# Performance work log

Measured on AMD Instinct MI355X. Metric: run time of the kernel, lower is better.

## Reference

```python
import jax, jax.numpy as jnp
import numpy as np

N_HEAD, D_MODEL, D_HEAD, D_OUT = 16, 1024, 64, 1024
Q_INNER = N_HEAD * D_HEAD


def setup_inputs() -> dict:
    key = jax.random.key(0)
    ks = jax.random.split(key, 10)
    B, S = 1, 4096
    hidden_state = jax.random.normal(ks[0], (B, S, D_MODEL), dtype=jnp.float32)
    # causal mask, (B,1,S,S), 1 = attend, 0 = masked
    attention_mask = jnp.tril(jnp.ones((S, S), dtype=jnp.int32))[None, None, :, :]
    s = 0.02
    Wq = jax.random.normal(ks[1], (D_MODEL, Q_INNER), dtype=jnp.float32) * s
    bq = jnp.zeros((Q_INNER,), dtype=jnp.float32)
    Wk = jax.random.normal(ks[2], (D_MODEL, D_HEAD), dtype=jnp.float32) * s
    bk = jnp.zeros((D_HEAD,), dtype=jnp.float32)
    Wv = jax.random.normal(ks[3], (D_MODEL, D_HEAD), dtype=jnp.float32) * s
    bv = jnp.zeros((D_HEAD,), dtype=jnp.float32)
    Wo = jax.random.normal(ks[4], (Q_INNER, D_OUT), dtype=jnp.float32) * s
    bo = jnp.zeros((D_OUT,), dtype=jnp.float32)
    return {"hidden_state": hidden_state, "attention_mask": attention_mask,
            "Wq": Wq, "bq": bq, "Wk": Wk, "bk": bk, "Wv": Wv, "bv": bv,
            "Wo": Wo, "bo": bo}


def reference(hidden_state, attention_mask, Wq, bq, Wk, bk, Wv, bv, Wo, bo):
    B, S, _ = hidden_state.shape
    q = hidden_state @ Wq + bq                    # (B,S,H*Dh)
    k = hidden_state @ Wk + bk                    # (B,S,Dh) single shared KV head
    v = hidden_state @ Wv + bv                    # (B,S,Dh)
    q = q.reshape(B, S, N_HEAD, D_HEAD)           # (B,S,H,Dh)
    scale = 1.0 / jnp.sqrt(jnp.float32(D_HEAD))
    # scores: (B,H,S,S) — shared K broadcast over heads
    scores = jnp.einsum('bqhd,bkd->bhqk', q, k) * scale
    scores = jnp.where(attention_mask == 0, -jnp.inf, scores)
    probs = jax.nn.softmax(scores, axis=-1)
    out = jnp.einsum('bhqk,bkd->bqhd', probs, v)  # (B,S,H,Dh)
    out = out.reshape(B, S, Q_INNER)
    return out @ Wo + bo
```

## Files before the change

### kernel.cpp

```cpp
#include <hip/hip_runtime.h>
#include <hip/hip_bf16.h>
#include <math.h>

typedef __bf16 bf16;
typedef __bf16 bf16x4 __attribute__((ext_vector_type(4)));
typedef __bf16 bf16x8 __attribute__((ext_vector_type(8)));
typedef float f32x4 __attribute__((ext_vector_type(4)));

#define AS1(p) ((const __attribute__((address_space(1))) void*)(p))
#define AS3(p) ((__attribute__((address_space(3))) void*)(p))

__device__ __forceinline__ void gld_lds16(const void* g, void* l) {
  __builtin_amdgcn_global_load_lds(AS1(g), AS3(l), 16, 0, 0);
}

#define MFMA16(a, b, c) __builtin_amdgcn_mfma_f32_16x16x32_bf16((a), (b), (c), 0, 0, 0)

#define QSCALE_F 0.180336880f


struct Sched { unsigned short e[768]; };
constexpr Sched make_sched() {
  Sched s{};
  for (int bx = 0; bx < 256; ++bx) {
    int h = bx >> 4, i = bx & 15;
    s.e[bx]       = (unsigned short)(((31 - i) << 6) | (h << 2) | 1);
    s.e[bx + 256] = (unsigned short)(((31 - i) << 6) | (h << 2) | 2);
    s.e[bx + 512] = (unsigned short)((i << 6) | (h << 2) | 0);
  }
  return s;
}
__device__ constexpr Sched SCHED = make_sched();

__global__ void cast_f32_bf16_sw(const float4* __restrict__ in, bf16* __restrict__ out,
                                 int n4) {
  int i = blockIdx.x * blockDim.x + threadIdx.x;
  if (i < n4) {
    float4 v = in[i];
    bf16x4 o4 = {(bf16)v.x, (bf16)v.y, (bf16)v.z, (bf16)v.w};
    const int e = i * 4;
    const int row = e >> 10;
    const int idx = (e & ~63) | ((e & 63) ^ ((row & 7) << 3));
    *(bf16x4*)(out + (size_t)idx) = o4;
  }
}

__global__ void prep_wqkv(const float* __restrict__ Wq, const float* __restrict__ Wk,
                          const float* __restrict__ Wv, bf16* __restrict__ out) {
  __shared__ float t[64][65];
  const int ob = blockIdx.y;
  const float* src;
  int C, c0;
  if (ob < 16)      { src = Wq; C = 1024; c0 = ob * 64; }
  else if (ob == 16){ src = Wk; C = 64;   c0 = 0; }
  else              { src = Wv; C = 64;   c0 = 0; }
  const int r0 = blockIdx.x * 64;
  const int tx = threadIdx.x & 63, ty = threadIdx.x >> 6;
#pragma unroll
  for (int j = 0; j < 16; j++)
    t[ty + j * 4][tx] = src[(size_t)(r0 + ty + j * 4) * C + c0 + tx];
  __syncthreads();
#pragma unroll
  for (int j = 0; j < 16; j++) {
    const int orow = ob * 64 + ty + j * 4;
    out[(size_t)orow * 1024 + r0 + (tx ^ ((orow & 7) << 3))] = (bf16)t[tx][ty + j * 4];
  }
}

__global__ void transpose_cast_sw(const float* __restrict__ in, bf16* __restrict__ out,
                                  int C, int ldout) {
  __shared__ float t[64][65];
  int r0 = blockIdx.y * 64, c0 = blockIdx.x * 64;
  int tx = threadIdx.x & 63, ty = threadIdx.x >> 6;
#pragma unroll
  for (int j = 0; j < 16; j++)
    t[ty + j * 4][tx] = in[(size_t)(r0 + ty + j * 4) * C + c0 + tx];
  __syncthreads();
#pragma unroll
  for (int j = 0; j < 16; j++) {
    const int orow = c0 + ty + j * 4;
    out[(size_t)orow * ldout + r0 + (tx ^ ((orow & 7) << 3))] = (bf16)t[tx][ty + j * 4];
  }
}

__global__ void pack_bias3(const float* __restrict__ bq, const float* __restrict__ bk,
                           const float* __restrict__ bv, float* __restrict__ o) {
  int i = blockIdx.x * 256 + threadIdx.x;
  if (i < 1024) o[i] = bq[i];
  else if (i < 1088) o[i] = bk[i - 1024];
  else if (i < 1152) o[i] = bv[i - 1088];
}

template <int OUTF32, int QSCALE>
__global__ __launch_bounds__(256) void gemm_bt64k(const bf16* __restrict__ A,
                                                  const bf16* __restrict__ B,
                                                  const float* __restrict__ bias,
                                                  void* __restrict__ Cout,
                                                  int M, int N, int K) {
  __shared__ bf16 As[2 * 64 * 64];
  __shared__ bf16 Bs[2 * 128 * 64];
  const int tid = threadIdx.x, w = tid >> 6, lane = tid & 63;
  const int g = lane >> 4, r = lane & 15;
  const int cpx = gridDim.x >> 3;
  const int l = (blockIdx.x & 7) * cpx + (blockIdx.x >> 3);
  const int ntn = N >> 7;
  const int my = l / ntn, mx = l - my * ntn;
  const int tm = my * 64, tn = mx * 128;
  const int wr = w >> 1, wc = w & 1;
  const int sz = (r & 7) << 4;

  f32x4 acc[2][4] = {};

  const char* gA = (const char*)(A + (size_t)tm * K);
  const char* gB = (const char*)(B + (size_t)tn * K);
  const int linA0 = (w * 2 + 0) * 1024 + lane * 16;
  const int linA1 = (w * 2 + 1) * 1024 + lane * 16;
  const int linB0 = (w * 4 + 0) * 1024 + lane * 16;
  const int linB1 = (w * 4 + 1) * 1024 + lane * 16;
  const int linB2 = (w * 4 + 2) * 1024 + lane * 16;
  const int linB3 = (w * 4 + 3) * 1024 + lane * 16;

  auto STAGE = [&](int ks, int b) {
    char* dA = (char*)As + b * 8192 + (w * 2) * 1024;
    char* dB = (char*)Bs + b * 16384 + (w * 4) * 1024;
    gld_lds16(gA + (size_t)(linA0 >> 7) * (K * 2) + ks * 128 + (linA0 & 127), dA);
    gld_lds16(gA + (size_t)(linA1 >> 7) * (K * 2) + ks * 128 + (linA1 & 127), dA + 1024);
    gld_lds16(gB + (size_t)(linB0 >> 7) * (K * 2) + ks * 128 + (linB0 & 127), dB);
    gld_lds16(gB + (size_t)(linB1 >> 7) * (K * 2) + ks * 128 + (linB1 & 127), dB + 1024);
    gld_lds16(gB + (size_t)(linB2 >> 7) * (K * 2) + ks * 128 + (linB2 & 127), dB + 2048);
    gld_lds16(gB + (size_t)(linB3 >> 7) * (K * 2) + ks * 128 + (linB3 & 127), dB + 3072);
  };

  const int nk = K >> 6;
  STAGE(0, 0);
  int buf = 0;
  for (int ks = 0; ks < nk; ++ks) {
    if (ks + 1 < nk) {
      STAGE(ks + 1, buf ^ 1);
      asm volatile("s_waitcnt vmcnt(6)" ::: "memory");
    } else {
      asm volatile("s_waitcnt vmcnt(0)" ::: "memory");
    }
    __builtin_amdgcn_sched_barrier(0);
    __builtin_amdgcn_s_barrier();

    const char* at = (const char*)As + buf * 8192;
    const char* bt = (const char*)Bs + buf * 16384;
    bf16x8 af[2][2], bfr[4][2];
#pragma unroll
    for (int m = 0; m < 2; m++)
#pragma unroll
      for (int kk = 0; kk < 2; kk++)
        af[m][kk] = *(const bf16x8*)(at + (wr * 32 + m * 16 + r) * 128 +
                                     ((kk * 64 + g * 16) ^ sz));
#pragma unroll
    for (int n = 0; n < 4; n++)
#pragma unroll
      for (int kk = 0; kk < 2; kk++)
        bfr[n][kk] = *(const bf16x8*)(bt + (wc * 64 + n * 16 + r) * 128 +
                                      ((kk * 64 + g * 16) ^ sz));
    __builtin_amdgcn_s_setprio(1);
#pragma unroll
    for (int m = 0; m < 2; m++)
#pragma unroll
      for (int n = 0; n < 4; n++) {
        acc[m][n] = MFMA16(af[m][0], bfr[n][0], acc[m][n]);
        acc[m][n] = MFMA16(af[m][1], bfr[n][1], acc[m][n]);
      }
    __builtin_amdgcn_s_setprio(0);
    __builtin_amdgcn_s_barrier();
    buf ^= 1;
  }

#pragma unroll
  for (int m = 0; m < 2; m++) {
#pragma unroll
    for (int n = 0; n < 4; n++) {
      int crow = tm + wr * 32 + m * 16 + g * 4;
      int ccol = tn + wc * 64 + n * 16 + r;
      float bb = bias[ccol];
      float sc = (QSCALE && ccol < 1024) ? QSCALE_F : 1.0f;
#pragma unroll
      for (int j = 0; j < 4; j++) {
        float v = (acc[m][n][j] + bb) * sc;
        if (OUTF32)
          ((float*)Cout)[(size_t)(crow + j) * N + ccol] = v;
        else
          ((bf16*)Cout)[(size_t)(crow + j) * N + ccol] = (bf16)v;
      }
    }
  }
}

__global__ void kv_prep(const bf16* __restrict__ QKV, bf16* __restrict__ Ksw,
                        bf16* __restrict__ Vtsw) {
  __shared__ bf16 Vld[64][72];
  const int kv0 = blockIdx.x * 64;
  const int tid = threadIdx.x;
#pragma unroll
  for (int cc = 0; cc < 2; cc++) {
    const int c = tid + cc * 256;
    const int kvl = c >> 3, c8 = c & 7;
    bf16x8 kv8 = *(const bf16x8*)(QKV + (size_t)(kv0 + kvl) * 1152 + 1024 + c8 * 8);
    *(bf16x8*)(Ksw + (size_t)(kv0 + kvl) * 64 + ((c8 * 8) ^ ((kvl & 7) << 3))) = kv8;
    bf16x8 vv = *(const bf16x8*)(QKV + (size_t)(kv0 + kvl) * 1152 + 1088 + c8 * 8);
#pragma unroll
    for (int e = 0; e < 8; e++) Vld[c8 * 8 + e][kvl] = vv[e];
  }
  __syncthreads();
#pragma unroll
  for (int cc = 0; cc < 2; cc++) {
    const int c = tid + cc * 256;
    const int d = c >> 3, k8 = c & 7;
    bf16x8 o8 = *(const bf16x8*)&Vld[d][k8 * 8];
    *(bf16x8*)(Vtsw + (size_t)d * 4096 + kv0 + ((k8 * 8) ^ ((d & 7) << 3))) = o8;
  }
}

__global__ __launch_bounds__(256) void mqa_fwd(const bf16* __restrict__ QKV,
                                               const bf16* __restrict__ Ksw,
                                               const bf16* __restrict__ Vtsw,
                                               bf16* __restrict__ AO,
                                               float* __restrict__ po,
                                               float* __restrict__ psum) {
  __shared__ bf16 Ks[2][64 * 64];
  __shared__ bf16 Vs[2][64 * 64];
  __shared__ bf16 Ps[4 * 32 * 64];

  const int e = SCHED.e[blockIdx.x];
  const int qt = e >> 6, h = (e >> 2) & 15, part = e & 3;
  const int tbeg = (part == 2) ? qt + 1 : 0;
  const int tend = (part == 1) ? qt + 1 : 2 * qt + 2;

  const int tid = threadIdx.x, w = tid >> 6, lane = tid & 63;
  const int g = lane >> 4, r = lane & 15;
  const int qw = qt * 128 + w * 32;
  const int qown0 = qw + r;
  const int qown1 = qw + 16 + r;

  const char* Kg = (const char*)Ksw;
  const char* Vg = (const char*)Vtsw;
  char* PsB = (char*)Ps;
  const int lin0 = w * 2048 + lane * 16;
  const int lin1 = lin0 + 1024;
  const int sz = (r & 7) << 4;

  bf16x8 qf0[2], qf1[2];
#pragma unroll
  for (int kk = 0; kk < 2; kk++) {
    qf0[kk] = *(const bf16x8*)&QKV[(size_t)qown0 * 1152 + h * 64 + kk * 32 + g * 8];
    qf1[kk] = *(const bf16x8*)&QKV[(size_t)qown1 * 1152 + h * 64 + kk * 32 + g * 8];
  }

  const bf16 one = (bf16)1.0f;
  const bf16x8 ones = {one, one, one, one, one, one, one, one};

  f32x4 o[2][4] = {};
  f32x4 sums[2] = {};

  auto STAGE = [&](int t, int b) {
    const int kn = t * 64;
    char* kb = (char*)Ks + b * 8192 + w * 2048;
    char* vb = (char*)Vs + b * 8192 + w * 2048;
    gld_lds16(Kg + (size_t)kn * 128 + lin0, kb);
    gld_lds16(Kg + (size_t)kn * 128 + lin1, kb + 1024);
    gld_lds16(Vg + (size_t)(lin0 >> 7) * 8192 + kn * 2 + (lin0 & 127), vb);
    gld_lds16(Vg + (size_t)(lin1 >> 7) * 8192 + kn * 2 + (lin1 & 127), vb + 1024);
  };

  int buf = 0;
  STAGE(tbeg, 0);
  for (int t = tbeg; t < tend; ++t) {
    if (t + 1 < tend) {
      STAGE(t + 1, buf ^ 1);
      asm volatile("s_waitcnt vmcnt(4)" ::: "memory");
    } else {
      asm volatile("s_waitcnt vmcnt(0)" ::: "memory");
    }
    __builtin_amdgcn_sched_barrier(0);
    __builtin_amdgcn_s_barrier();

    const char* kt = (const char*)Ks + buf * 8192;
    const char* vt = (const char*)Vs + buf * 8192;
    const int kv0 = t * 64;

    f32x4 s0[4], s1[4];
    __builtin_amdgcn_s_setprio(1);
#pragma unroll
    for (int n = 0; n < 4; n++) {
      bf16x8 kf0 = *(const bf16x8*)(kt + (n * 16 + r) * 128 + ((g * 16) ^ sz));
      bf16x8 kf1 = *(const bf16x8*)(kt + (n * 16 + r) * 128 + ((64 + g * 16) ^ sz));
      f32x4 z0 = {0.f, 0.f, 0.f, 0.f};
      z0 = MFMA16(kf0, qf0[0], z0);
      z0 = MFMA16(kf1, qf0[1], z0);
      s0[n] = z0;
      f32x4 z1 = {0.f, 0.f, 0.f, 0.f};
      z1 = MFMA16(kf0, qf1[0], z1);
      z1 = MFMA16(kf1, qf1[1], z1);
      s1[n] = z1;
    }
    __builtin_amdgcn_s_setprio(0);

    if (t >= 2 * qt) {
#pragma unroll
      for (int n = 0; n < 4; n++)
#pragma unroll
        for (int jj = 0; jj < 4; jj++) {
          const int kv = kv0 + n * 16 + g * 4 + jj;
          if (kv > qown0) s0[n][jj] = -3.0e38f;
          if (kv > qown1) s1[n][jj] = -3.0e38f;
        }
    }

#pragma unroll
    for (int n = 0; n < 4; n++) {
      bf16x4 pk0, pk1;
#pragma unroll
      for (int jj = 0; jj < 4; jj++) {
        pk0[jj] = (bf16)__builtin_amdgcn_exp2f(s0[n][jj]);
        pk1[jj] = (bf16)__builtin_amdgcn_exp2f(s1[n][jj]);
      }
      *(bf16x4*)(PsB + w * 4096 + r * 128 + ((n * 32 + g * 8) ^ sz)) = pk0;
      *(bf16x4*)(PsB + w * 4096 + (16 + r) * 128 + ((n * 32 + g * 8) ^ sz)) = pk1;
    }

    asm volatile("s_waitcnt lgkmcnt(0)" ::: "memory");
    __builtin_amdgcn_sched_barrier(0);

    bf16x8 pa00 = *(const bf16x8*)(PsB + w * 4096 + r * 128 + ((g * 16) ^ sz));
    bf16x8 pa01 = *(const bf16x8*)(PsB + w * 4096 + r * 128 + ((64 + g * 16) ^ sz));
    bf16x8 pa10 = *(const bf16x8*)(PsB + w * 4096 + (16 + r) * 128 + ((g * 16) ^ sz));
    bf16x8 pa11 = *(const bf16x8*)(PsB + w * 4096 + (16 + r) * 128 + ((64 + g * 16) ^ sz));
    __builtin_amdgcn_s_setprio(1);
    sums[0] = MFMA16(pa00, ones, sums[0]);
    sums[0] = MFMA16(pa01, ones, sums[0]);
    sums[1] = MFMA16(pa10, ones, sums[1]);
    sums[1] = MFMA16(pa11, ones, sums[1]);
#pragma unroll
    for (int n = 0; n < 4; n++) {
      bf16x8 vf0 = *(const bf16x8*)(vt + (n * 16 + r) * 128 + ((g * 16) ^ sz));
      bf16x8 vf1 = *(const bf16x8*)(vt + (n * 16 + r) * 128 + ((64 + g * 16) ^ sz));
      o[0][n] = MFMA16(pa00, vf0, o[0][n]);
      o[0][n] = MFMA16(pa01, vf1, o[0][n]);
      o[1][n] = MFMA16(pa10, vf0, o[1][n]);
      o[1][n] = MFMA16(pa11, vf1, o[1][n]);
    }
    __builtin_amdgcn_s_setprio(0);
    __builtin_amdgcn_s_barrier();
    buf ^= 1;
  }

  if (part == 0) {
#pragma unroll
    for (int H = 0; H < 2; H++)
#pragma unroll
      for (int jj = 0; jj < 4; jj++) {
        const float inv = 1.f / sums[H][jj];
        const int row = qw + H * 16 + g * 4 + jj;
        const int key = (row & 7) << 3;
#pragma unroll
        for (int n = 0; n < 4; n++)
          AO[(size_t)row * 1024 + h * 64 + ((n * 16 + r) ^ key)] =
              (bf16)(o[H][n][jj] * inv);
      }
  } else {
    const int slot = ((qt - 16) * 16 + h) * 2 + (part - 1);
    float* pb = po + (size_t)slot * 8192;
#pragma unroll
    for (int H = 0; H < 2; H++)
#pragma unroll
      for (int jj = 0; jj < 4; jj++) {
        const int row = w * 32 + H * 16 + g * 4 + jj;
#pragma unroll
        for (int n = 0; n < 4; n++)
          pb[row * 64 + n * 16 + r] = o[H][n][jj];
        if (r == 0) psum[slot * 128 + row] = sums[H][jj];
      }
  }
}

__global__ __launch_bounds__(256) void combine_split(const float* __restrict__ po,
                                                     const float* __restrict__ psum,
                                                     bf16* __restrict__ AO) {
  const int bxx = blockIdx.x;
  const int qt = 16 + (bxx >> 4), h = bxx & 15;
  const float* a  = po + (size_t)bxx * 16384;
  const float* b  = a + 8192;
  const float* sa = psum + bxx * 256;
  const float* sb = sa + 128;
  const int row = threadIdx.x >> 1, c0 = (threadIdx.x & 1) * 32;
  const float inv = 1.f / (sa[row] + sb[row]);
  const float* pa = a + row * 64 + c0;
  const float* pb = b + row * 64 + c0;
  const int grow = qt * 128 + row;
  const int key = (grow & 7) << 3;
  bf16* dst = AO + (size_t)grow * 1024 + h * 64;
#pragma unroll
  for (int i = 0; i < 8; i++) {
    float4 va = ((const float4*)pa)[i];
    float4 vb = ((const float4*)pb)[i];
    bf16x4 o4 = {(bf16)((va.x + vb.x) * inv), (bf16)((va.y + vb.y) * inv),
                 (bf16)((va.z + vb.z) * inv), (bf16)((va.w + vb.w) * inv)};
    *(bf16x4*)(dst + ((c0 + i * 4) ^ key)) = o4;
  }
}

extern "C" void kernel_launch(void* const* d_in, const int* in_sizes, int n_in,
                              void* d_out, int out_size, void* d_ws, size_t ws_size,
                              hipStream_t stream) {
  const float* H  = (const float*)d_in[0];
  const float* Wq = (const float*)d_in[2];
  const float* bq = (const float*)d_in[3];
  const float* Wk = (const float*)d_in[4];
  const float* bk = (const float*)d_in[5];
  const float* Wv = (const float*)d_in[6];
  const float* bv = (const float*)d_in[7];
  const float* Wo = (const float*)d_in[8];
  const float* bo = (const float*)d_in[9];
  float* out = (float*)d_out;

  const int S = 4096, DM = 1024;

  char* p = (char*)d_ws;
  bf16* Hb    = (bf16*)(p);
  bf16* QKV   = (bf16*)(p + 8388608);
  bf16* Wqkvt = (bf16*)(p + 17825792);
  bf16* Wot   = (bf16*)(p + 20185088);
  float* bqkv = (float*)(p + 22282240);
  bf16* Ksw   = (bf16*)(p + 22286848);
  bf16* Vtsw  = (bf16*)(p + 22811136);
  float* po   = (float*)(p + 23335424);
  float* psum = (float*)(p + 40112640);
  bf16* AOb   = Hb;

  cast_f32_bf16_sw<<<(S * DM / 4 + 255) / 256, 256, 0, stream>>>((const float4*)H, Hb,
                                                                 S * DM / 4);
  prep_wqkv<<<dim3(16, 18), 256, 0, stream>>>(Wq, Wk, Wv, Wqkvt);
  transpose_cast_sw<<<dim3(16, 16), 256, 0, stream>>>(Wo, Wot, 1024, 1024);
  pack_bias3<<<5, 256, 0, stream>>>(bq, bk, bv, bqkv);

  gemm_bt64k<0, 1><<<576, 256, 0, stream>>>(Hb, Wqkvt, bqkv, QKV, S, 1152, 1024);

  kv_prep<<<64, 256, 0, stream>>>(QKV, Ksw, Vtsw);

  mqa_fwd<<<768, 256, 0, stream>>>(QKV, Ksw, Vtsw, AOb, po, psum);
  combine_split<<<256, 256, 0, stream>>>(po, psum, AOb);

  gemm_bt64k<1, 0><<<512, 256, 0, stream>>>(AOb, Wot, bo, out, S, 1024, 1024);
}
```

Before: 118.2 us.

## Balance causal attention work with variable-length KV splits and bf16 partials

Replaces the fixed two-way split of the upper query tiles with a compile-time work tape that cuts every (query tile, head) row into chunks of at most 22 KV tiles, ordered longest first. This gives 1008 blocks of more even size so the GPU tail at the end of the grid is shorter. The combine kernel now sums a variable number of partial outputs per tile. Those partials are stored as bf16 instead of fp32 to halve their traffic, which costs some accuracy in the unnormalized partial sums.

```diff
diff --git a/kernel.cpp b/kernel.cpp
--- a/kernel.cpp
+++ b/kernel.cpp
@@ -19,18 +19,48 @@
 #define QSCALE_F 0.180336880f
 
 
-struct Sched { unsigned short e[768]; };
-constexpr Sched make_sched() {
-  Sched s{};
-  for (int bx = 0; bx < 256; ++bx) {
-    int h = bx >> 4, i = bx & 15;
-    s.e[bx]       = (unsigned short)(((31 - i) << 6) | (h << 2) | 1);
-    s.e[bx + 256] = (unsigned short)(((31 - i) << 6) | (h << 2) | 2);
-    s.e[bx + 512] = (unsigned short)((i << 6) | (h << 2) | 0);
-  }
-  return s;
-}
-__device__ constexpr Sched SCHED = make_sched();
+struct Seg { short qt, h, t0, t1, slot; };
+struct Tape { Seg s[1008]; };
+struct CJob { short qt, h, base, parts; };
+struct CTab { CJob j[336]; };
+
+constexpr int nparts_of(int qt) { int T = 2 * qt + 2; return (T + 21) / 22; }
+constexpr int slot_base(int h, int qt) {
+  int b = h * 52;
+  if (qt <= 21) return b + (qt - 11) * 2;
+  return b + 22 + (qt - 22) * 3;
+}
+
+constexpr Tape make_tape() {
+  Tape tp{};
+  int idx = 0;
+  for (int s = 22; s >= 1; --s)
+    for (int h = 0; h < 16; ++h)
+      for (int qt = 0; qt < 32; ++qt) {
+        const int T = 2 * qt + 2, P = nparts_of(qt);
+        for (int p = 0; p < P; ++p) {
+          const int a = p * T / P, b = (p + 1) * T / P;
+          if (b - a == s) {
+            const int slot = (P == 1) ? -1 : slot_base(h, qt) + p;
+            tp.s[idx++] = Seg{(short)qt, (short)h, (short)a, (short)b, (short)slot};
+          }
+        }
+      }
+  return tp;
+}
+
+constexpr CTab make_ctab() {
+  CTab ct{};
+  int n = 0;
+  for (int h = 0; h < 16; ++h)
+    for (int qt = 11; qt < 32; ++qt)
+      ct.j[n++] = CJob{(short)qt, (short)h, (short)slot_base(h, qt),
+                       (short)nparts_of(qt)};
+  return ct;
+}
+
+__device__ constexpr Tape TAPE = make_tape();
+__device__ constexpr CTab CTAB = make_ctab();
 
 __global__ void cast_f32_bf16_sw(const float4* __restrict__ in, bf16* __restrict__ out,
                                  int n4) {
@@ -221,16 +251,14 @@
                                                const bf16* __restrict__ Ksw,
                                                const bf16* __restrict__ Vtsw,
                                                bf16* __restrict__ AO,
-                                               float* __restrict__ po,
+                                               bf16* __restrict__ po,
                                                float* __restrict__ psum) {
   __shared__ bf16 Ks[2][64 * 64];
   __shared__ bf16 Vs[2][64 * 64];
   __shared__ bf16 Ps[4 * 32 * 64];
 
-  const int e = SCHED.e[blockIdx.x];
-  const int qt = e >> 6, h = (e >> 2) & 15, part = e & 3;
-  const int tbeg = (part == 2) ? qt + 1 : 0;
-  const int tend = (part == 1) ? qt + 1 : 2 * qt + 2;
+  const Seg sg = TAPE.s[blockIdx.x];
+  const int qt = sg.qt, h = sg.h, tbeg = sg.t0, tend = sg.t1, slot = sg.slot;
 
   const int tid = threadIdx.x, w = tid >> 6, lane = tid & 63;
   const int g = lane >> 4, r = lane & 15;
@@ -350,7 +378,7 @@
     buf ^= 1;
   }
 
-  if (part == 0) {
+  if (slot < 0) {
 #pragma unroll
     for (int H = 0; H < 2; H++)
 #pragma unroll
@@ -364,8 +392,7 @@
               (bf16)(o[H][n][jj] * inv);
       }
   } else {
-    const int slot = ((qt - 16) * 16 + h) * 2 + (part - 1);
-    float* pb = po + (size_t)slot * 8192;
+    bf16* pb = po + (size_t)slot * 8192;
 #pragma unroll
     for (int H = 0; H < 2; H++)
 #pragma unroll
@@ -373,34 +400,38 @@
         const int row = w * 32 + H * 16 + g * 4 + jj;
 #pragma unroll
         for (int n = 0; n < 4; n++)
-          pb[row * 64 + n * 16 + r] = o[H][n][jj];
+          pb[row * 64 + n * 16 + r] = (bf16)o[H][n][jj];
         if (r == 0) psum[slot * 128 + row] = sums[H][jj];
       }
   }
 }
 
-__global__ __launch_bounds__(256) void combine_split(const float* __restrict__ po,
+__global__ __launch_bounds__(256) void combine_split(const bf16* __restrict__ po,
                                                      const float* __restrict__ psum,
                                                      bf16* __restrict__ AO) {
-  const int bxx = blockIdx.x;
-  const int qt = 16 + (bxx >> 4), h = bxx & 15;
-  const float* a  = po + (size_t)bxx * 16384;
-  const float* b  = a + 8192;
-  const float* sa = psum + bxx * 256;
-  const float* sb = sa + 128;
+  const CJob cj = CTAB.j[blockIdx.x];
   const int row = threadIdx.x >> 1, c0 = (threadIdx.x & 1) * 32;
-  const float inv = 1.f / (sa[row] + sb[row]);
-  const float* pa = a + row * 64 + c0;
-  const float* pb = b + row * 64 + c0;
-  const int grow = qt * 128 + row;
+  float acc[32] = {};
+  float ssum = 0.f;
+#pragma unroll 1
+  for (int p = 0; p < cj.parts; ++p) {
+    const bf16* pb = po + (size_t)(cj.base + p) * 8192 + row * 64 + c0;
+    ssum += psum[(cj.base + p) * 128 + row];
+#pragma unroll
+    for (int v = 0; v < 4; ++v) {
+      bf16x8 x = ((const bf16x8*)pb)[v];
+#pragma unroll
+      for (int e = 0; e < 8; e++) acc[v * 8 + e] += (float)x[e];
+    }
+  }
+  const float inv = 1.f / ssum;
+  const int grow = cj.qt * 128 + row;
   const int key = (grow & 7) << 3;
-  bf16* dst = AO + (size_t)grow * 1024 + h * 64;
+  bf16* dst = AO + (size_t)grow * 1024 + cj.h * 64;
 #pragma unroll
   for (int i = 0; i < 8; i++) {
-    float4 va = ((const float4*)pa)[i];
-    float4 vb = ((const float4*)pb)[i];
-    bf16x4 o4 = {(bf16)((va.x + vb.x) * inv), (bf16)((va.y + vb.y) * inv),
-                 (bf16)((va.z + vb.z) * inv), (bf16)((va.w + vb.w) * inv)};
+    bf16x4 o4 = {(bf16)(acc[i * 4 + 0] * inv), (bf16)(acc[i * 4 + 1] * inv),
+                 (bf16)(acc[i * 4 + 2] * inv), (bf16)(acc[i * 4 + 3] * inv)};
     *(bf16x4*)(dst + ((c0 + i * 4) ^ key)) = o4;
   }
 }
@@ -429,8 +460,8 @@
   float* bqkv = (float*)(p + 22282240);
   bf16* Ksw   = (bf16*)(p + 22286848);
   bf16* Vtsw  = (bf16*)(p + 22811136);
-  float* po   = (float*)(p + 23335424);
-  float* psum = (float*)(p + 40112640);
+  bf16* po    = (bf16*)(p + 23335424);
+  float* psum = (float*)(p + 36966912);
   bf16* AOb   = Hb;
 
   cast_f32_bf16_sw<<<(S * DM / 4 + 255) / 256, 256, 0, stream>>>((const float4*)H, Hb,
@@ -443,8 +474,8 @@
 
   kv_prep<<<64, 256, 0, stream>>>(QKV, Ksw, Vtsw);
 
-  mqa_fwd<<<768, 256, 0, stream>>>(QKV, Ksw, Vtsw, AOb, po, psum);
-  combine_split<<<256, 256, 0, stream>>>(po, psum, AOb);
+  mqa_fwd<<<1008, 256, 0, stream>>>(QKV, Ksw, Vtsw, AOb, po, psum);
+  combine_split<<<336, 256, 0, stream>>>(po, psum, AOb);
 
   gemm_bt64k<1, 0><<<512, 256, 0, stream>>>(AOb, Wot, bo, out, S, 1024, 1024);
 }
```

Measured after the change: 119.9 us. Within noise of the previous version (+1.5%).

## Feed P from registers into K=16 MFMA, dropping LDS round-trip for probabilities

Applied to the files above, without the earlier changes.

Replaces the LDS write/read of the softmax probabilities with a register-resident path. The 16x16x32 MFMA output layout is consumed directly as the A operand of the 16x16x16 bf16_1k MFMA. This removes the Ps shared buffer, one waitcnt/sched barrier and per-tile LDS traffic, and reduces LDS footprint so launch_bounds can request 3 blocks per SIMD. In exchange it issues twice as many MFMA instructions, each with half the K, and loads V fragments in smaller 4-element pieces, which adds register pressure.

```diff
diff --git a/kernel.cpp b/kernel.cpp
--- a/kernel.cpp
+++ b/kernel.cpp
@@ -6,6 +6,7 @@
 typedef __bf16 bf16x4 __attribute__((ext_vector_type(4)));
 typedef __bf16 bf16x8 __attribute__((ext_vector_type(8)));
 typedef float f32x4 __attribute__((ext_vector_type(4)));
+typedef short s16x4 __attribute__((ext_vector_type(4)));
 
 #define AS1(p) ((const __attribute__((address_space(1))) void*)(p))
 #define AS3(p) ((__attribute__((address_space(3))) void*)(p))
@@ -15,6 +16,7 @@
 }
 
 #define MFMA16(a, b, c) __builtin_amdgcn_mfma_f32_16x16x32_bf16((a), (b), (c), 0, 0, 0)
+#define MFMA16K(a, b, c) __builtin_amdgcn_mfma_f32_16x16x16bf16_1k((a), (b), (c), 0, 0, 0)
 
 #define QSCALE_F 0.180336880f
 
@@ -217,15 +219,14 @@
   }
 }
 
-__global__ __launch_bounds__(256) void mqa_fwd(const bf16* __restrict__ QKV,
-                                               const bf16* __restrict__ Ksw,
-                                               const bf16* __restrict__ Vtsw,
-                                               bf16* __restrict__ AO,
-                                               float* __restrict__ po,
-                                               float* __restrict__ psum) {
+__global__ __launch_bounds__(256, 3) void mqa_fwd(const bf16* __restrict__ QKV,
+                                                  const bf16* __restrict__ Ksw,
+                                                  const bf16* __restrict__ Vtsw,
+                                                  bf16* __restrict__ AO,
+                                                  float* __restrict__ po,
+                                                  float* __restrict__ psum) {
   __shared__ bf16 Ks[2][64 * 64];
   __shared__ bf16 Vs[2][64 * 64];
-  __shared__ bf16 Ps[4 * 32 * 64];
 
   const int e = SCHED.e[blockIdx.x];
   const int qt = e >> 6, h = (e >> 2) & 15, part = e & 3;
@@ -240,7 +241,6 @@
 
   const char* Kg = (const char*)Ksw;
   const char* Vg = (const char*)Vtsw;
-  char* PsB = (char*)Ps;
   const int lin0 = w * 2048 + lane * 16;
   const int lin1 = lin0 + 1024;
   const int sz = (r & 7) << 4;
@@ -252,11 +252,9 @@
     qf1[kk] = *(const bf16x8*)&QKV[(size_t)qown1 * 1152 + h * 64 + kk * 32 + g * 8];
   }
 
-  const bf16 one = (bf16)1.0f;
-  const bf16x8 ones = {one, one, one, one, one, one, one, one};
-
   f32x4 o[2][4] = {};
   f32x4 sums[2] = {};
+  const s16x4 ones4 = {0x3F80, 0x3F80, 0x3F80, 0x3F80};
 
   auto STAGE = [&](int t, int b) {
     const int kn = t * 64;
@@ -301,6 +299,14 @@
     }
     __builtin_amdgcn_s_setprio(0);
 
+    s16x4 vf[4][4];
+#pragma unroll
+    for (int kb = 0; kb < 4; kb++)
+#pragma unroll
+      for (int n = 0; n < 4; n++)
+        vf[kb][n] = *(const s16x4*)(vt + (n * 16 + r) * 128 +
+                                    ((kb * 32 + g * 8) ^ sz));
+
     if (t >= 2 * qt) {
 #pragma unroll
       for (int n = 0; n < 4; n++)
@@ -312,38 +318,26 @@
         }
     }
 
-#pragma unroll
-    for (int n = 0; n < 4; n++) {
-      bf16x4 pk0, pk1;
+    union PW { bf16x4 hh; s16x4 ss; };
+    PW p0[4], p1[4];
+#pragma unroll
+    for (int n = 0; n < 4; n++)
 #pragma unroll
       for (int jj = 0; jj < 4; jj++) {
-        pk0[jj] = (bf16)__builtin_amdgcn_exp2f(s0[n][jj]);
-        pk1[jj] = (bf16)__builtin_amdgcn_exp2f(s1[n][jj]);
-      }
-      *(bf16x4*)(PsB + w * 4096 + r * 128 + ((n * 32 + g * 8) ^ sz)) = pk0;
-      *(bf16x4*)(PsB + w * 4096 + (16 + r) * 128 + ((n * 32 + g * 8) ^ sz)) = pk1;
-    }
-
-    asm volatile("s_waitcnt lgkmcnt(0)" ::: "memory");
-    __builtin_amdgcn_sched_barrier(0);
-
-    bf16x8 pa00 = *(const bf16x8*)(PsB + w * 4096 + r * 128 + ((g * 16) ^ sz));
-    bf16x8 pa01 = *(const bf16x8*)(PsB + w * 4096 + r * 128 + ((64 + g * 16) ^ sz));
-    bf16x8 pa10 = *(const bf16x8*)(PsB + w * 4096 + (16 + r) * 128 + ((g * 16) ^ sz));
-    bf16x8 pa11 = *(const bf16x8*)(PsB + w * 4096 + (16 + r) * 128 + ((64 + g * 16) ^ sz));
+        p0[n].hh[jj] = (bf16)__builtin_amdgcn_exp2f(s0[n][jj]);
+        p1[n].hh[jj] = (bf16)__builtin_amdgcn_exp2f(s1[n][jj]);
+      }
+
     __builtin_amdgcn_s_setprio(1);
-    sums[0] = MFMA16(pa00, ones, sums[0]);
-    sums[0] = MFMA16(pa01, ones, sums[0]);
-    sums[1] = MFMA16(pa10, ones, sums[1]);
-    sums[1] = MFMA16(pa11, ones, sums[1]);
-#pragma unroll
-    for (int n = 0; n < 4; n++) {
-      bf16x8 vf0 = *(const bf16x8*)(vt + (n * 16 + r) * 128 + ((g * 16) ^ sz));
-      bf16x8 vf1 = *(const bf16x8*)(vt + (n * 16 + r) * 128 + ((64 + g * 16) ^ sz));
-      o[0][n] = MFMA16(pa00, vf0, o[0][n]);
-      o[0][n] = MFMA16(pa01, vf1, o[0][n]);
-      o[1][n] = MFMA16(pa10, vf0, o[1][n]);
-      o[1][n] = MFMA16(pa11, vf1, o[1][n]);
+#pragma unroll
+    for (int kb = 0; kb < 4; kb++) {
+      sums[0] = MFMA16K(p0[kb].ss, ones4, sums[0]);
+      sums[1] = MFMA16K(p1[kb].ss, ones4, sums[1]);
+#pragma unroll
+      for (int n = 0; n < 4; n++) {
+        o[0][n] = MFMA16K(p0[kb].ss, vf[kb][n], o[0][n]);
+        o[1][n] = MFMA16K(p1[kb].ss, vf[kb][n], o[1][n]);
+      }
     }
     __builtin_amdgcn_s_setprio(0);
     __builtin_amdgcn_s_barrier();
```

New measurement: 117.7 us. About the same (-0.4%).
